# Optimization experiments

Hardware: AMD Instinct MI355X
Metric: run time of the kernel (lower is better)

Reference implementation:

```python
import jax, jax.numpy as jnp
import numpy as np

N_NODES = 50000
N_EDGES = 800000


def setup_inputs() -> dict:
    key = jax.random.key(0)
    k1, k2, k3, k4 = jax.random.split(key, 4)
    x = jax.random.normal(k1, (N_NODES, 100), dtype=jnp.float32)
    edge_index = jax.random.randint(k2, (2, N_EDGES), 0, N_NODES, dtype=jnp.int64)
    W1 = jax.random.normal(k3, (100, 128), dtype=jnp.float32) * 0.1
    b1 = jnp.zeros((128,), dtype=jnp.float32)
    W2 = jax.random.normal(k4, (128, 64), dtype=jnp.float32) * 0.1
    b2 = jnp.zeros((64,), dtype=jnp.float32)
    return {"x": x, "edge_index": edge_index, "W1": W1, "b1": b1, "W2": W2, "b2": b2}


def _gcn_norm(edge_index, n_nodes):
    # PyG GCNConv default: add self-loops, then symmetric normalization
    row, col = edge_index[0], edge_index[1]
    loop = jnp.arange(n_nodes, dtype=row.dtype)
    row = jnp.concatenate([row, loop])
    col = jnp.concatenate([col, loop])
    deg = jax.ops.segment_sum(jnp.ones_like(col, dtype=jnp.float32), col,
                              num_segments=n_nodes)
    dinv = jnp.where(deg > 0, jax.lax.rsqrt(deg), 0.0)
    norm = dinv[row] * dinv[col]  # [E + N]
    return row, col, norm


def _gcn_conv(x, W, b, row, col, norm, n_nodes):
    h = x @ W                       # [N, out] linear transform first (PyG order)
    msg = norm[:, None] * h[row]    # gather + scale over edges
    agg = jax.ops.segment_sum(msg, col, num_segments=n_nodes)  # scatter-add
    return agg + b


def reference(x, edge_index, W1, b1, W2, b2):
    n = x.shape[0]
    row, col, norm = _gcn_norm(edge_index, n)
    h = _gcn_conv(x, W1, b1, row, col, norm, n)
    h = jax.nn.relu(h)
    out = _gcn_conv(h, W2, b2, row, col, norm, n)
    return out
```

## Files before the change

### kernel.cpp

```cpp
#include <hip/hip_runtime.h>
#include <hip/hip_fp16.h>

#define DIV_UP(a,b) (((a)+(b)-1)/(b))

typedef _Float16 half8 __attribute__((ext_vector_type(8)));
typedef float f32x4 __attribute__((ext_vector_type(4)));

#define BUK_BITS 8
#define BUK_SIZE 256
#define BUK_CAP  6144
#define CSR_CAP  8192
#define MAXBUK   256
#define NBLK_BUCKET 256
#define CHUNK_MAX 3136

#define SWZ(row, colh) ((colh) ^ (((row) & 7) << 3))


__device__ __forceinline__ int edge_at(const void* ei, int mode64, int idx) {
  if (mode64) return (int)((const long long*)ei)[idx];
  return ((const int*)ei)[idx];
}

__global__ __launch_bounds__(256) void k_init(const int* __restrict__ ei32,
                                              int* __restrict__ mode,
                                              int* __restrict__ bcur, int nbuk,
                                              const float* __restrict__ W1,
                                              const float* __restrict__ W2,
                                              _Float16* __restrict__ Wt1,
                                              _Float16* __restrict__ Wt2) {
  int t = threadIdx.x;
  if (blockIdx.x == 0) {
    if (t < 64) {
      int v = ei32[2 * t + 1];
      unsigned long long b = __ballot(v == 0);
      if (t == 0) *mode = (b == ~0ull) ? 1 : 0;
    }
    if (t < nbuk) bcur[t] = t * BUK_CAP;
  } else {
    int i = (blockIdx.x - 1) * 256 + t;
    if (i < 128 * 128) {
      int nn = i >> 7, k = i & 127;
      Wt1[i] = (k < 100) ? (_Float16)W1[k * 128 + nn] : (_Float16)0.f;
    } else {
      int j = i - 128 * 128;
      int nn = j >> 7, k = j & 127;
      Wt2[j] = (_Float16)W2[k * 64 + nn];
    }
  }
}

__global__ __launch_bounds__(256) void k_bucket(const void* __restrict__ ei,
                                                const int* __restrict__ mode,
                                                int* __restrict__ bcur,
                                                unsigned int* __restrict__ recs,
                                                int E, int nbuk) {
  __shared__ unsigned int lrec[CHUNK_MAX];
  __shared__ unsigned int sorted[CHUNK_MAX];
  __shared__ int hist[MAXBUK], lofs[MAXBUK], gbase[MAXBUK], cur[MAXBUK];

  const int chunk = DIV_UP(E, gridDim.x);
  const int e0 = blockIdx.x * chunk;
  const int cnt = min(E, e0 + chunk) - e0;
  if (cnt <= 0) return;

  for (int i = threadIdx.x; i < nbuk; i += 256) hist[i] = 0;
  __syncthreads();

  const int m = *mode;
  for (int i = threadIdx.x; i < cnt; i += 256) {
    int r = edge_at(ei, m, e0 + i);
    int c = edge_at(ei, m, E + e0 + i);
    unsigned int rec = ((unsigned)c << 16) | (unsigned)r;
    lrec[i] = rec;
    atomicAdd(&hist[c >> BUK_BITS], 1);
  }
  __syncthreads();

  if (threadIdx.x == 0) {
    int run = 0;
    for (int b = 0; b < nbuk; ++b) { lofs[b] = run; run += hist[b]; }
  }
  __syncthreads();
  for (int b = threadIdx.x; b < nbuk; b += 256) {
    gbase[b] = atomicAdd(&bcur[b], hist[b]);
    cur[b] = lofs[b];
  }
  __syncthreads();

  for (int i = threadIdx.x; i < cnt; i += 256) {
    unsigned int rec = lrec[i];
    int b = rec >> (16 + BUK_BITS);
    int p = atomicAdd(&cur[b], 1);
    sorted[p] = rec;
  }
  __syncthreads();

  for (int i = threadIdx.x; i < cnt; i += 256) {
    unsigned int rec = sorted[i];
    int b = rec >> (16 + BUK_BITS);
    recs[gbase[b] + i - lofs[b]] = rec;
  }
}

__global__ __launch_bounds__(256) void k_bdeg_fill(const int* __restrict__ bcur,
                                                   const unsigned int* __restrict__ recs,
                                                   float* __restrict__ dinv,
                                                   int2* __restrict__ rowinfo,
                                                   unsigned short* __restrict__ csr,
                                                   int n) {
  __shared__ int h[BUK_SIZE];
  __shared__ int psum[BUK_SIZE];
  __shared__ int curs[BUK_SIZE];
  __shared__ unsigned short lcsr[CSR_CAP];

  const int b = blockIdx.x, tid = threadIdx.x;
  const int base = b * BUK_CAP;
  const int cnt = bcur[b] - base;
  const int n0 = b << BUK_BITS;
  const int nn = min(BUK_SIZE, n - n0);

  h[tid] = 0;
  __syncthreads();
  for (int i = tid; i < cnt; i += 256)
    atomicAdd(&h[(int)(recs[base + i] >> 16) - n0], 1);
  __syncthreads();

  const int deg = h[tid];
  const int plen = (deg + 7) & ~7;
  psum[tid] = plen;
  __syncthreads();
#pragma unroll
  for (int off2 = 1; off2 < 256; off2 <<= 1) {
    int v = (tid >= off2) ? psum[tid - off2] : 0;
    __syncthreads();
    psum[tid] += v;
    __syncthreads();
  }
  const int excl = psum[tid] - plen;
  const int ptot = psum[255];

  if (tid < nn) {
    rowinfo[n0 + tid] = make_int2(b * CSR_CAP + excl, plen);
    dinv[n0 + tid] = rsqrtf((float)deg + 1.0f);
    curs[tid] = excl;
  }
  for (int i = tid; i < ptot; i += 256) lcsr[i] = (unsigned short)n;
  __syncthreads();

  for (int i = tid; i < cnt; i += 256) {
    unsigned int rec = recs[base + i];
    int cl = (int)(rec >> 16) - n0;
    int p = atomicAdd(&curs[cl], 1);
    lcsr[p] = (unsigned short)(rec & 0xFFFFu);
  }
  __syncthreads();
  for (int i = tid; i < ptot; i += 256) csr[b * CSR_CAP + i] = lcsr[i];
}

__global__ __launch_bounds__(256) void k_convx(const float4* __restrict__ x4,
                                               const float* __restrict__ dinv,
                                               uint2* __restrict__ xh4,
                                               uint2* __restrict__ thh2,
                                               int n, int total) {
  int i = blockIdx.x * 256 + threadIdx.x;
  if (i < total) {
    int node = i >> 5;
    int lane = i & 31;
    if (node < n && lane < 25) {
      float d = dinv[node];
      float4 v = x4[node * 25 + lane];
      union { uint2 u; __half2 h[2]; } p;
      p.h[0] = __halves2half2(__float2half_rn(d * v.x), __float2half_rn(d * v.y));
      p.h[1] = __halves2half2(__float2half_rn(d * v.z), __float2half_rn(d * v.w));
      xh4[i] = p.u;
    } else {
      xh4[i] = make_uint2(0u, 0u);
    }
  } else {
    int s = i - total;
    if (s < 16) thh2[n * 16 + s] = make_uint2(0u, 0u);
  }
}

__device__ __forceinline__ float4 h4_to_f4(uint2 u) {
  union { uint2 u; __half2 h[2]; } p; p.u = u;
  float2 a = __half22float2(p.h[0]);
  float2 b = __half22float2(p.h[1]);
  return make_float4(a.x, a.y, b.x, b.y);
}
__device__ __forceinline__ void acc_add(float4& acc, float4 a) {
  acc.x += a.x; acc.y += a.y; acc.z += a.z; acc.w += a.w;
}

__global__ __launch_bounds__(256) void k_pull1(const int2* __restrict__ rowinfo,
                                               const unsigned short* __restrict__ csr,
                                               const uint2* __restrict__ xh4,
                                               const float* __restrict__ dinv,
                                               uint2* __restrict__ aggh4, int n) {
  const int b = blockIdx.x;
  const int slice = (b & 7) >> 1;
  const int g = ((b >> 3) << 1) + (b & 1);
  const int node = g * 32 + (threadIdx.x >> 3);
  const int lane = threadIdx.x & 7;
  if (node >= n) return;
  const int so = slice * 8 + lane;

  float4 acc = h4_to_f4(xh4[(node << 5) + so]);
  int2 ri = rowinfo[node];
  int beg = ri.x, end = ri.x + ri.y;
  for (int j = beg; j < end; j += 8) {
    uint4 cw = *(const uint4*)&csr[j];
    int r0 = cw.x & 0xFFFF, r1 = cw.x >> 16;
    int r2 = cw.y & 0xFFFF, r3 = cw.y >> 16;
    int r4 = cw.z & 0xFFFF, r5 = cw.z >> 16;
    int r6 = cw.w & 0xFFFF, r7 = cw.w >> 16;
    float4 t0 = h4_to_f4(xh4[(r0 << 5) + so]);
    float4 t1 = h4_to_f4(xh4[(r1 << 5) + so]);
    float4 t2 = h4_to_f4(xh4[(r2 << 5) + so]);
    float4 t3 = h4_to_f4(xh4[(r3 << 5) + so]);
    float4 t4 = h4_to_f4(xh4[(r4 << 5) + so]);
    float4 t5 = h4_to_f4(xh4[(r5 << 5) + so]);
    float4 t6 = h4_to_f4(xh4[(r6 << 5) + so]);
    float4 t7 = h4_to_f4(xh4[(r7 << 5) + so]);
    acc_add(acc, t0); acc_add(acc, t1); acc_add(acc, t2); acc_add(acc, t3);
    acc_add(acc, t4); acc_add(acc, t5); acc_add(acc, t6); acc_add(acc, t7);
  }
  float d = dinv[node];
  union { uint2 u; __half2 h[2]; } p;
  p.h[0] = __halves2half2(__float2half_rn(d * acc.x), __float2half_rn(d * acc.y));
  p.h[1] = __halves2half2(__float2half_rn(d * acc.z), __float2half_rn(d * acc.w));
  aggh4[(node << 5) + so] = p.u;
}

__global__ __launch_bounds__(256) void k_pull2(const int2* __restrict__ rowinfo,
                                               const unsigned short* __restrict__ csr,
                                               const uint2* __restrict__ th2,
                                               const float* __restrict__ dinv,
                                               const float4* __restrict__ b2_4,
                                               float4* __restrict__ out4, int n) {
  const int b = blockIdx.x;
  const int slice = (b & 7) >> 2;
  const int g = ((b >> 3) << 2) + (b & 3);
  const int node = g * 32 + (threadIdx.x >> 3);
  const int lane = threadIdx.x & 7;
  if (node >= n) return;
  const int so = slice * 8 + lane;

  float4 acc = h4_to_f4(th2[(node << 4) + so]);
  int2 ri = rowinfo[node];
  int beg = ri.x, end = ri.x + ri.y;
  for (int j = beg; j < end; j += 8) {
    uint4 cw = *(const uint4*)&csr[j];
    int r0 = cw.x & 0xFFFF, r1 = cw.x >> 16;
    int r2 = cw.y & 0xFFFF, r3 = cw.y >> 16;
    int r4 = cw.z & 0xFFFF, r5 = cw.z >> 16;
    int r6 = cw.w & 0xFFFF, r7 = cw.w >> 16;
    float4 t0 = h4_to_f4(th2[(r0 << 4) + so]);
    float4 t1 = h4_to_f4(th2[(r1 << 4) + so]);
    float4 t2 = h4_to_f4(th2[(r2 << 4) + so]);
    float4 t3 = h4_to_f4(th2[(r3 << 4) + so]);
    float4 t4 = h4_to_f4(th2[(r4 << 4) + so]);
    float4 t5 = h4_to_f4(th2[(r5 << 4) + so]);
    float4 t6 = h4_to_f4(th2[(r6 << 4) + so]);
    float4 t7 = h4_to_f4(th2[(r7 << 4) + so]);
    acc_add(acc, t0); acc_add(acc, t1); acc_add(acc, t2); acc_add(acc, t3);
    acc_add(acc, t4); acc_add(acc, t5); acc_add(acc, t6); acc_add(acc, t7);
  }
  float d = dinv[node];
  float4 bb = b2_4[so];
  out4[(node << 4) + so] = make_float4(d * acc.x + bb.x, d * acc.y + bb.y,
                                       d * acc.z + bb.z, d * acc.w + bb.w);
}

__global__ __launch_bounds__(256, 2) void k_gemmf(const _Float16* __restrict__ A,
                                                  const _Float16* __restrict__ Wt1,
                                                  const float* __restrict__ b1,
                                                  const _Float16* __restrict__ Wt2,
                                                  const float* __restrict__ dinv,
                                                  _Float16* __restrict__ thh, int n) {
  __shared__ __align__(16) _Float16 lds[4][16 * 128];
  const int wid = threadIdx.x >> 6;
  const int lane = threadIdx.x & 63;
  const int lr = lane & 15;
  const int lk = lane >> 4;
  _Float16* myl = lds[wid];

  half8 B1[8][4];
#pragma unroll
  for (int nt = 0; nt < 8; ++nt)
#pragma unroll
    for (int ks = 0; ks < 4; ++ks)
      B1[nt][ks] = *(const half8*)&Wt1[(nt * 16 + lr) * 128 + ks * 32 + lk * 8];
  float bs[8];
#pragma unroll
  for (int nt = 0; nt < 8; ++nt) bs[nt] = b1[nt * 16 + lr];

  const int nstrips = (n + 15) >> 4;
  for (int s = blockIdx.x * 4 + wid; s < nstrips; s += gridDim.x * 4) {
    const int arow = s * 16 + lr;
    half8 a[4];
#pragma unroll
    for (int ks = 0; ks < 4; ++ks)
      a[ks] = (arow < n) ? *(const half8*)&A[(size_t)arow * 128 + ks * 32 + lk * 8]
                         : half8{0, 0, 0, 0, 0, 0, 0, 0};
    f32x4 acc[8];
#pragma unroll
    for (int nt = 0; nt < 8; ++nt) acc[nt] = f32x4{0.f, 0.f, 0.f, 0.f};
#pragma unroll
    for (int ks = 0; ks < 4; ++ks)
#pragma unroll
      for (int nt = 0; nt < 8; ++nt)
        acc[nt] = __builtin_amdgcn_mfma_f32_16x16x32_f16(a[ks], B1[nt][ks], acc[nt], 0, 0, 0);

#pragma unroll
    for (int r = 0; r < 4; ++r) {
      int row = lk * 4 + r;
#pragma unroll
      for (int nt = 0; nt < 8; ++nt)
        myl[row * 128 + SWZ(row, nt * 16 + lr)] =
            (_Float16)fmaxf(acc[nt][r] + bs[nt], 0.f);
    }

    half8 B2[4][4];
#pragma unroll
    for (int nt = 0; nt < 4; ++nt)
#pragma unroll
      for (int ks = 0; ks < 4; ++ks)
        B2[nt][ks] = *(const half8*)&Wt2[(nt * 16 + lr) * 128 + ks * 32 + lk * 8];

    half8 a2[4];
#pragma unroll
    for (int ks = 0; ks < 4; ++ks)
      a2[ks] = *(const half8*)&myl[lr * 128 + SWZ(lr, ks * 32 + lk * 8)];

    f32x4 acc2[4];
#pragma unroll
    for (int nt = 0; nt < 4; ++nt) acc2[nt] = f32x4{0.f, 0.f, 0.f, 0.f};
#pragma unroll
    for (int ks = 0; ks < 4; ++ks)
#pragma unroll
      for (int nt = 0; nt < 4; ++nt)
        acc2[nt] = __builtin_amdgcn_mfma_f32_16x16x32_f16(a2[ks], B2[nt][ks], acc2[nt], 0, 0, 0);

    const int rb = s * 16 + lk * 4;
    float sc[4];
    if (rb + 3 < n) {
      const float4 dv = *(const float4*)&dinv[rb];
      sc[0] = dv.x; sc[1] = dv.y; sc[2] = dv.z; sc[3] = dv.w;
    } else {
#pragma unroll
      for (int r = 0; r < 4; ++r) sc[r] = (rb + r < n) ? dinv[rb + r] : 0.f;
    }
#pragma unroll
    for (int r = 0; r < 4; ++r) {
      const int orow = rb + r;
      if (orow < n) {
#pragma unroll
        for (int nt = 0; nt < 4; ++nt)
          thh[(size_t)orow * 64 + nt * 16 + lr] = (_Float16)(acc2[nt][r] * sc[r]);
      }
    }
  }
}

extern "C" void kernel_launch(void* const* d_in, const int* in_sizes, int n_in,
                              void* d_out, int out_size, void* d_ws, size_t ws_size,
                              hipStream_t stream) {
  const float* x  = (const float*)d_in[0];
  const void*  ei = d_in[1];
  const float* W1 = (const float*)d_in[2];
  const float* b1 = (const float*)d_in[3];
  const float* W2 = (const float*)d_in[4];
  const float* b2 = (const float*)d_in[5];
  float* out = (float*)d_out;

  const int n = in_sizes[0] / 100;
  const int E = in_sizes[1] / 2;
  const int nbuk = DIV_UP(n, BUK_SIZE);

  char* ws = (char*)d_ws;
  size_t off = 0;
  auto alloc = [&](size_t bytes) { void* p = ws + off; off += (bytes + 15) & ~15ull; return p; };
  int*            mode     = (int*)   alloc(64 * 4);
  int*            bcur     = (int*)   alloc(MAXBUK * 4);
  float*          dinv     = (float*) alloc((size_t)n * 4);
  int2*           rowinfo  = (int2*)  alloc((size_t)n * 8);
  unsigned int*   recs     = (unsigned int*)alloc((size_t)nbuk * BUK_CAP * 4);
  unsigned short* csr      = (unsigned short*)alloc((size_t)nbuk * CSR_CAP * 2);
  _Float16*       xh       = (_Float16*)alloc((size_t)(n + 1) * 128 * 2);
  _Float16*       aggh     = (_Float16*)alloc((size_t)n * 128 * 2);
  _Float16*       thh      = (_Float16*)alloc((size_t)(n + 1) * 64 * 2);
  _Float16*       Wt1h     = (_Float16*)alloc(128 * 128 * 2);
  _Float16*       Wt2h     = (_Float16*)alloc(64 * 128 * 2);

  k_init<<<97, 256, 0, stream>>>((const int*)ei, mode, bcur, nbuk, W1, W2, Wt1h, Wt2h);
  k_bucket<<<NBLK_BUCKET, 256, 0, stream>>>(ei, mode, bcur, recs, E, nbuk);
  k_bdeg_fill<<<nbuk, 256, 0, stream>>>(bcur, recs, dinv, rowinfo, csr, n);

  const int total = (n + 1) * 32;
  k_convx<<<DIV_UP(total + 16, 256), 256, 0, stream>>>((const float4*)x, dinv,
      (uint2*)xh, (uint2*)thh, n, total);

  const int ngroups = DIV_UP(n, 32);
  k_pull1<<<DIV_UP(ngroups, 2) * 8, 256, 0, stream>>>(rowinfo, csr, (const uint2*)xh,
                                                      dinv, (uint2*)aggh, n);
  const int nstrips = DIV_UP(n, 16);
  k_gemmf<<<DIV_UP(nstrips, 8), 256, 0, stream>>>(aggh, Wt1h, b1, Wt2h, dinv, thh, n);
  k_pull2<<<DIV_UP(ngroups, 4) * 8, 256, 0, stream>>>(rowinfo, csr, (const uint2*)thh,
                                                      dinv, (const float4*)b2,
                                                      (float4*)out, n);
}
```

Before: 120.7 us.

## Fuse x conversion into degree fill and schedule pull slices per XCC

Folds the fp16 conversion and dinv scaling of x into k_bdeg_fill, removing the separate k_convx launch. The two pull kernels now take work through per-slice atomic counters, and each block starts on the slice picked by its XCC ID, so each XCD's L2 sees only a narrow column slice of the gathered features. CSR loads and the output stores become nontemporal. The risks are atomic claim overhead, serialisation on a single thread per block, and reliance on the XCC hardware register.

```diff
diff --git a/kernel.cpp b/kernel.cpp
--- a/kernel.cpp
+++ b/kernel.cpp
@@ -5,6 +5,8 @@
 
 typedef _Float16 half8 __attribute__((ext_vector_type(8)));
 typedef float f32x4 __attribute__((ext_vector_type(4)));
+typedef unsigned int u32x4 __attribute__((ext_vector_type(4)));
+typedef unsigned int u32x2 __attribute__((ext_vector_type(2)));
 
 #define BUK_BITS 8
 #define BUK_SIZE 256
@@ -14,17 +16,26 @@
 #define NBLK_BUCKET 256
 #define CHUNK_MAX 3136
 
+#define NSL1 8
+#define NSL2 4
+
 #define SWZ(row, colh) ((colh) ^ (((row) & 7) << 3))
-
 
 __device__ __forceinline__ int edge_at(const void* ei, int mode64, int idx) {
   if (mode64) return (int)((const long long*)ei)[idx];
   return ((const int*)ei)[idx];
 }
 
+__device__ __forceinline__ int get_xcc() {
+  int x;
+  asm volatile("s_getreg_b32 %0, hwreg(HW_REG_XCC_ID)" : "=s"(x));
+  return x & 7;
+}
+
 __global__ __launch_bounds__(256) void k_init(const int* __restrict__ ei32,
                                               int* __restrict__ mode,
                                               int* __restrict__ bcur, int nbuk,
+                                              int* __restrict__ pcur,
                                               const float* __restrict__ W1,
                                               const float* __restrict__ W2,
                                               _Float16* __restrict__ Wt1,
@@ -37,6 +48,7 @@
       if (t == 0) *mode = (b == ~0ull) ? 1 : 0;
     }
     if (t < nbuk) bcur[t] = t * BUK_CAP;
+    if (t >= 224 && t < 224 + NSL1 + NSL2) pcur[t - 224] = 0;
   } else {
     int i = (blockIdx.x - 1) * 256 + t;
     if (i < 128 * 128) {
@@ -105,9 +117,12 @@
 
 __global__ __launch_bounds__(256) void k_bdeg_fill(const int* __restrict__ bcur,
                                                    const unsigned int* __restrict__ recs,
+                                                   const float4* __restrict__ x4,
                                                    float* __restrict__ dinv,
                                                    int2* __restrict__ rowinfo,
                                                    unsigned short* __restrict__ csr,
+                                                   uint2* __restrict__ xh4,
+                                                   uint2* __restrict__ thh2,
                                                    int n) {
   __shared__ int h[BUK_SIZE];
   __shared__ int psum[BUK_SIZE];
@@ -156,30 +171,24 @@
   }
   __syncthreads();
   for (int i = tid; i < ptot; i += 256) csr[b * CSR_CAP + i] = lcsr[i];
-}
-
-__global__ __launch_bounds__(256) void k_convx(const float4* __restrict__ x4,
-                                               const float* __restrict__ dinv,
-                                               uint2* __restrict__ xh4,
-                                               uint2* __restrict__ thh2,
-                                               int n, int total) {
-  int i = blockIdx.x * 256 + threadIdx.x;
-  if (i < total) {
-    int node = i >> 5;
-    int lane = i & 31;
-    if (node < n && lane < 25) {
-      float d = dinv[node];
+
+  for (int i = tid; i < nn * 32; i += 256) {
+    int nl = i >> 5, lane = i & 31;
+    int node = n0 + nl;
+    uint2 val = make_uint2(0u, 0u);
+    if (lane < 25) {
+      float d = rsqrtf((float)h[nl] + 1.0f);
       float4 v = x4[node * 25 + lane];
-      union { uint2 u; __half2 h[2]; } p;
-      p.h[0] = __halves2half2(__float2half_rn(d * v.x), __float2half_rn(d * v.y));
-      p.h[1] = __halves2half2(__float2half_rn(d * v.z), __float2half_rn(d * v.w));
-      xh4[i] = p.u;
-    } else {
-      xh4[i] = make_uint2(0u, 0u);
-    }
-  } else {
-    int s = i - total;
-    if (s < 16) thh2[n * 16 + s] = make_uint2(0u, 0u);
+      union { uint2 u; __half2 hh[2]; } p;
+      p.hh[0] = __halves2half2(__float2half_rn(d * v.x), __float2half_rn(d * v.y));
+      p.hh[1] = __halves2half2(__float2half_rn(d * v.z), __float2half_rn(d * v.w));
+      val = p.u;
+    }
+    xh4[(node << 5) + lane] = val;
+  }
+  if (b == 0) {
+    if (tid < 32) xh4[(n << 5) + tid] = make_uint2(0u, 0u);
+    else if (tid < 48) thh2[(n << 4) + (tid - 32)] = make_uint2(0u, 0u);
   }
 }
 
@@ -189,28 +198,45 @@
   float2 b = __half22float2(p.h[1]);
   return make_float4(a.x, a.y, b.x, b.y);
 }
+__device__ __forceinline__ float4 h4_to_f4u(u32x2 u) {
+  return h4_to_f4(make_uint2(u.x, u.y));
+}
 __device__ __forceinline__ void acc_add(float4& acc, float4 a) {
   acc.x += a.x; acc.y += a.y; acc.z += a.z; acc.w += a.w;
+}
+
+__device__ __forceinline__ void claim(int* __restrict__ cur, int nsl, int pref,
+                                      int ngroups, int* sg) {
+  int s = 0, g = 0;
+  for (int k = 0; k < nsl; ++k) {
+    s = pref + k; if (s >= nsl) s -= nsl;
+    g = atomicAdd(&cur[s], 1);
+    if (g < ngroups) break;
+  }
+  sg[0] = s; sg[1] = g;
 }
 
 __global__ __launch_bounds__(256) void k_pull1(const int2* __restrict__ rowinfo,
                                                const unsigned short* __restrict__ csr,
                                                const uint2* __restrict__ xh4,
                                                const float* __restrict__ dinv,
-                                               uint2* __restrict__ aggh4, int n) {
-  const int b = blockIdx.x;
-  const int slice = (b & 7) >> 1;
-  const int g = ((b >> 3) << 1) + (b & 1);
-  const int node = g * 32 + (threadIdx.x >> 3);
-  const int lane = threadIdx.x & 7;
+                                               unsigned int* __restrict__ aggh2,
+                                               int* __restrict__ cur,
+                                               int ngroups, int n) {
+  __shared__ int sg[2];
+  if (threadIdx.x == 0) claim(cur, NSL1, get_xcc(), ngroups, sg);
+  __syncthreads();
+  const int slice = sg[0];
+  const int node = sg[1] * 64 + (threadIdx.x >> 2);
+  const int lane = threadIdx.x & 3;
   if (node >= n) return;
-  const int so = slice * 8 + lane;
+  const int so = slice * 4 + lane;
 
   float4 acc = h4_to_f4(xh4[(node << 5) + so]);
   int2 ri = rowinfo[node];
   int beg = ri.x, end = ri.x + ri.y;
   for (int j = beg; j < end; j += 8) {
-    uint4 cw = *(const uint4*)&csr[j];
+    u32x4 cw = __builtin_nontemporal_load((const u32x4*)&csr[j]);
     int r0 = cw.x & 0xFFFF, r1 = cw.x >> 16;
     int r2 = cw.y & 0xFFFF, r3 = cw.y >> 16;
     int r4 = cw.z & 0xFFFF, r5 = cw.z >> 16;
@@ -227,10 +253,10 @@
     acc_add(acc, t4); acc_add(acc, t5); acc_add(acc, t6); acc_add(acc, t7);
   }
   float d = dinv[node];
-  union { uint2 u; __half2 h[2]; } p;
+  union { u32x2 u; __half2 h[2]; } p;
   p.h[0] = __halves2half2(__float2half_rn(d * acc.x), __float2half_rn(d * acc.y));
   p.h[1] = __halves2half2(__float2half_rn(d * acc.z), __float2half_rn(d * acc.w));
-  aggh4[(node << 5) + so] = p.u;
+  __builtin_nontemporal_store(p.u, (u32x2*)&aggh2[((node << 5) + so) * 2]);
 }
 
 __global__ __launch_bounds__(256) void k_pull2(const int2* __restrict__ rowinfo,
@@ -238,20 +264,23 @@
                                                const uint2* __restrict__ th2,
                                                const float* __restrict__ dinv,
                                                const float4* __restrict__ b2_4,
-                                               float4* __restrict__ out4, int n) {
-  const int b = blockIdx.x;
-  const int slice = (b & 7) >> 2;
-  const int g = ((b >> 3) << 2) + (b & 3);
-  const int node = g * 32 + (threadIdx.x >> 3);
-  const int lane = threadIdx.x & 7;
+                                               float* __restrict__ outf,
+                                               int* __restrict__ cur,
+                                               int ngroups, int n) {
+  __shared__ int sg[2];
+  if (threadIdx.x == 0) claim(cur, NSL2, get_xcc() >> 1, ngroups, sg);
+  __syncthreads();
+  const int slice = sg[0];
+  const int node = sg[1] * 64 + (threadIdx.x >> 2);
+  const int lane = threadIdx.x & 3;
   if (node >= n) return;
-  const int so = slice * 8 + lane;
+  const int so = slice * 4 + lane;
 
   float4 acc = h4_to_f4(th2[(node << 4) + so]);
   int2 ri = rowinfo[node];
   int beg = ri.x, end = ri.x + ri.y;
   for (int j = beg; j < end; j += 8) {
-    uint4 cw = *(const uint4*)&csr[j];
+    u32x4 cw = __builtin_nontemporal_load((const u32x4*)&csr[j]);
     int r0 = cw.x & 0xFFFF, r1 = cw.x >> 16;
     int r2 = cw.y & 0xFFFF, r3 = cw.y >> 16;
     int r4 = cw.z & 0xFFFF, r5 = cw.z >> 16;
@@ -269,8 +298,8 @@
   }
   float d = dinv[node];
   float4 bb = b2_4[so];
-  out4[(node << 4) + so] = make_float4(d * acc.x + bb.x, d * acc.y + bb.y,
-                                       d * acc.z + bb.z, d * acc.w + bb.w);
+  f32x4 o = {d * acc.x + bb.x, d * acc.y + bb.y, d * acc.z + bb.z, d * acc.w + bb.w};
+  __builtin_nontemporal_store(o, (f32x4*)&outf[((node << 4) + so) * 4]);
 }
 
 __global__ __launch_bounds__(256, 2) void k_gemmf(const _Float16* __restrict__ A,
@@ -384,6 +413,7 @@
   auto alloc = [&](size_t bytes) { void* p = ws + off; off += (bytes + 15) & ~15ull; return p; };
   int*            mode     = (int*)   alloc(64 * 4);
   int*            bcur     = (int*)   alloc(MAXBUK * 4);
+  int*            pcur     = (int*)   alloc((NSL1 + NSL2) * 4);
   float*          dinv     = (float*) alloc((size_t)n * 4);
   int2*           rowinfo  = (int2*)  alloc((size_t)n * 8);
   unsigned int*   recs     = (unsigned int*)alloc((size_t)nbuk * BUK_CAP * 4);
@@ -394,20 +424,18 @@
   _Float16*       Wt1h     = (_Float16*)alloc(128 * 128 * 2);
   _Float16*       Wt2h     = (_Float16*)alloc(64 * 128 * 2);
 
-  k_init<<<97, 256, 0, stream>>>((const int*)ei, mode, bcur, nbuk, W1, W2, Wt1h, Wt2h);
+  k_init<<<97, 256, 0, stream>>>((const int*)ei, mode, bcur, nbuk, pcur,
+                                 W1, W2, Wt1h, Wt2h);
   k_bucket<<<NBLK_BUCKET, 256, 0, stream>>>(ei, mode, bcur, recs, E, nbuk);
-  k_bdeg_fill<<<nbuk, 256, 0, stream>>>(bcur, recs, dinv, rowinfo, csr, n);
-
-  const int total = (n + 1) * 32;
-  k_convx<<<DIV_UP(total + 16, 256), 256, 0, stream>>>((const float4*)x, dinv,
-      (uint2*)xh, (uint2*)thh, n, total);
-
-  const int ngroups = DIV_UP(n, 32);
-  k_pull1<<<DIV_UP(ngroups, 2) * 8, 256, 0, stream>>>(rowinfo, csr, (const uint2*)xh,
-                                                      dinv, (uint2*)aggh, n);
+  k_bdeg_fill<<<nbuk, 256, 0, stream>>>(bcur, recs, (const float4*)x, dinv,
+                                        rowinfo, csr, (uint2*)xh, (uint2*)thh, n);
+
+  const int ngroups = DIV_UP(n, 64);
+  k_pull1<<<NSL1 * ngroups, 256, 0, stream>>>(rowinfo, csr, (const uint2*)xh, dinv,
+                                              (unsigned int*)aggh, pcur, ngroups, n);
   const int nstrips = DIV_UP(n, 16);
   k_gemmf<<<DIV_UP(nstrips, 8), 256, 0, stream>>>(aggh, Wt1h, b1, Wt2h, dinv, thh, n);
-  k_pull2<<<DIV_UP(ngroups, 4) * 8, 256, 0, stream>>>(rowinfo, csr, (const uint2*)thh,
-                                                      dinv, (const float4*)b2,
-                                                      (float4*)out, n);
-}
+  k_pull2<<<NSL2 * ngroups, 256, 0, stream>>>(rowinfo, csr, (const uint2*)thh, dinv,
+                                              (const float4*)b2, out,
+                                              pcur + NSL1, ngroups, n);
+}
```

After: 304.3 us. +152.0%, slower.
